# Performance work log

Hardware: AMD Instinct MI355X
Metric: run time of the kernel (lower is better)

Reference implementation:

```python
import jax, jax.numpy as jnp
import numpy as np

TOP_K = 2

def _expert(x, w1, w2, w3):
    return (jax.nn.silu(x @ w1.T) * (x @ w3.T)) @ w2.T

def setup_inputs() -> dict:
    key = jax.random.key(0)
    ks = jax.random.split(key, 8)
    B, L, D, F, E, S = 4, 2048, 1024, 512, 16, 1
    p = lambda k, shape: (jax.random.normal(k, shape, jnp.float32) * 0.02)
    return {
        "x": jax.random.normal(ks[0], (B, L, D), jnp.float32),
        "gate_w": p(ks[1], (E, D)),
        "expert_bias": jnp.zeros((E,), jnp.float32),
        "sw1": p(ks[2], (S, F, D)),
        "sw2": p(ks[3], (S, D, F)),
        "sw3": p(ks[4], (S, F, D)),
        "ew1": p(ks[5], (E, F, D)),
        "ew2": p(ks[6], (E, D, F)),
        "ew3": p(ks[7], (E, F, D)),
    }

def reference(x, gate_w, expert_bias, sw1, sw2, sw3, ew1, ew2, ew3):
    B, L, D = x.shape
    E = gate_w.shape[0]
    flat_x = x.reshape(-1, D)  # [T, D], T = B*L

    # Shared experts (always-on)
    shared = sum(_expert(flat_x, sw1[i], sw2[i], sw3[i]) for i in range(sw1.shape[0]))

    # Router (eval mode: no jitter noise, no bias update; expert_bias buffer added)
    logits = flat_x @ gate_w.T + expert_bias          # [T, E]
    probs = jax.nn.softmax(logits, axis=-1)
    topw, topi = jax.lax.top_k(probs, TOP_K)          # [T, k]
    topw = topw / jnp.sum(topw, axis=-1, keepdims=True)

    # Routed experts: combine weight per (token, expert); zero weight => zero contribution,
    # identical math to the masked gather/scatter in the original.
    out = jnp.zeros_like(flat_x)
    for e in range(E):  # fixed small structural loop over experts
        cw = jnp.sum(jnp.where(topi == e, topw, 0.0), axis=-1)  # [T]
        out = out + cw[:, None] * _expert(flat_x, ew1[e], ew2[e], ew3[e])

    y = (shared + out).reshape(B, L, D)
    return y, probs
```

## Files before the change

### kernel.cpp

```cpp
#include <hip/hip_runtime.h>

typedef unsigned short u16;
typedef __bf16 bf16_t;
typedef bf16_t bf16x8 __attribute__((ext_vector_type(8)));
typedef float f32x4 __attribute__((ext_vector_type(4)));

#define T_TOK 8192
#define DIM   1024
#define FF    512
#define NE    16
#define RBASE_SHARED (2 * T_TOK)
#define NROWS (RBASE_SHARED + T_TOK)
#define MAXTILES 256
#define NSEG 512

__device__ __forceinline__ u16 f2bf(float f) {
  union { float f; unsigned u; } v; v.f = f;
  unsigned r = v.u + 0x7FFFu + ((v.u >> 16) & 1u);
  return (u16)(r >> 16);
}
__device__ __forceinline__ float bf2f(u16 h) {
  union { unsigned u; float f; } v; v.u = ((unsigned)h) << 16; return v.f;
}
__device__ __forceinline__ int clampi(int v, int lo, int hi) {
  return v < lo ? lo : (v > hi ? hi : v);
}

#define GLL16(g, l) __builtin_amdgcn_global_load_lds( \
    (const __attribute__((address_space(1))) void*)(g), \
    (__attribute__((address_space(3))) void*)(l), 16, 0, 0)

#define X4   2097152
#define SW4  131072
#define EW4  2097152
#define TOT4 (X4 + 3 * SW4 + 3 * EW4)

__global__ __launch_bounds__(256) void cvt_all_kernel(
    const float* __restrict__ x, const float* __restrict__ sw1,
    const float* __restrict__ sw2, const float* __restrict__ sw3,
    const float* __restrict__ ew1, const float* __restrict__ ew2,
    const float* __restrict__ ew3,
    u16* __restrict__ xb, u16* __restrict__ sw1b, u16* __restrict__ sw2b,
    u16* __restrict__ sw3b, u16* __restrict__ ew1b, u16* __restrict__ ew2b,
    u16* __restrict__ ew3b) {
  int i = blockIdx.x * 256 + threadIdx.x;
  const float* s; u16* dst; int j;
  if (i < X4)                       { s = x;   dst = xb;   j = i; }
  else if (i < X4 + SW4)            { s = sw1; dst = sw1b; j = i - X4; }
  else if (i < X4 + 2 * SW4)        { s = sw2; dst = sw2b; j = i - (X4 + SW4); }
  else if (i < X4 + 3 * SW4)        { s = sw3; dst = sw3b; j = i - (X4 + 2 * SW4); }
  else if (i < X4 + 3 * SW4 + EW4)      { s = ew1; dst = ew1b; j = i - (X4 + 3 * SW4); }
  else if (i < X4 + 3 * SW4 + 2 * EW4)  { s = ew2; dst = ew2b; j = i - (X4 + 3 * SW4 + EW4); }
  else if (i < TOT4)                    { s = ew3; dst = ew3b; j = i - (X4 + 3 * SW4 + 2 * EW4); }
  else return;
  float4 v = reinterpret_cast<const float4*>(s)[j];
  ushort4 o;
  o.x = f2bf(v.x); o.y = f2bf(v.y); o.z = f2bf(v.z); o.w = f2bf(v.w);
  reinterpret_cast<ushort4*>(dst)[j] = o;
}

__global__ __launch_bounds__(256) void router_kernel(
    const float* __restrict__ x, const float* __restrict__ gw,
    const float* __restrict__ ebias, float* __restrict__ probs,
    int* __restrict__ topi, float* __restrict__ topw, int* __restrict__ cnt_seg) {
  __shared__ int hist[16];
  int tid = threadIdx.x;
  int lane = tid & 63, w = tid >> 6;
  if (tid < 16) hist[tid] = 0;
  __syncthreads();
  const float4* gv = reinterpret_cast<const float4*>(gw);
  for (int it = 0; it < 2; ++it) {
    int t0 = blockIdx.x * 16 + (w + 4 * it) * 2;
    const float4* x0 = reinterpret_cast<const float4*>(x + (size_t)t0 * DIM);
    const float4* x1 = reinterpret_cast<const float4*>(x + (size_t)(t0 + 1) * DIM);
    float4 xa[4], xc[4];
#pragma unroll
    for (int j = 0; j < 4; ++j) { xa[j] = x0[j * 64 + lane]; xc[j] = x1[j * 64 + lane]; }
    float p0[16], p1[16];
#pragma unroll
    for (int e = 0; e < NE; ++e) {
      float s0 = 0.f, s1 = 0.f;
#pragma unroll
      for (int j = 0; j < 4; ++j) {
        float4 g = gv[e * 256 + j * 64 + lane];
        s0 += xa[j].x * g.x + xa[j].y * g.y + xa[j].z * g.z + xa[j].w * g.w;
        s1 += xc[j].x * g.x + xc[j].y * g.y + xc[j].z * g.z + xc[j].w * g.w;
      }
#pragma unroll
      for (int d = 1; d < 64; d <<= 1) { s0 += __shfl_xor(s0, d); s1 += __shfl_xor(s1, d); }
      float b = ebias[e];
      p0[e] = s0 + b; p1[e] = s1 + b;
    }
    float m0 = p0[0], m1 = p1[0];
#pragma unroll
    for (int e = 1; e < NE; ++e) { m0 = fmaxf(m0, p0[e]); m1 = fmaxf(m1, p1[e]); }
    float sum0 = 0.f, sum1 = 0.f;
#pragma unroll
    for (int e = 0; e < NE; ++e) {
      p0[e] = __expf(p0[e] - m0); sum0 += p0[e];
      p1[e] = __expf(p1[e] - m1); sum1 += p1[e];
    }
    float inv0 = 1.f / sum0, inv1 = 1.f / sum1;
#pragma unroll
    for (int e = 0; e < NE; ++e) { p0[e] *= inv0; p1[e] *= inv1; }
    if (lane == 0) {
#pragma unroll
      for (int j = 0; j < 4; ++j)
        reinterpret_cast<float4*>(probs + (size_t)t0 * NE)[j] =
            make_float4(p0[4 * j], p0[4 * j + 1], p0[4 * j + 2], p0[4 * j + 3]);
      float b1 = -1.f, b2 = -1.f; int i1 = 0, i2 = 0;
#pragma unroll
      for (int e = 0; e < NE; ++e) {
        float pe = p0[e];
        if (pe > b1) { b2 = b1; i2 = i1; b1 = pe; i1 = e; }
        else if (pe > b2) { b2 = pe; i2 = e; }
      }
      float ws = b1 + b2;
      reinterpret_cast<int2*>(topi)[t0] = make_int2(i1, i2);
      reinterpret_cast<float2*>(topw)[t0] = make_float2(b1 / ws, b2 / ws);
      atomicAdd(&hist[i1], 1); atomicAdd(&hist[i2], 1);
    }
    if (lane == 1) {
      int t1 = t0 + 1;
#pragma unroll
      for (int j = 0; j < 4; ++j)
        reinterpret_cast<float4*>(probs + (size_t)t1 * NE)[j] =
            make_float4(p1[4 * j], p1[4 * j + 1], p1[4 * j + 2], p1[4 * j + 3]);
      float b1 = -1.f, b2 = -1.f; int i1 = 0, i2 = 0;
#pragma unroll
      for (int e = 0; e < NE; ++e) {
        float pe = p1[e];
        if (pe > b1) { b2 = b1; i2 = i1; b1 = pe; i1 = e; }
        else if (pe > b2) { b2 = pe; i2 = e; }
      }
      float ws = b1 + b2;
      reinterpret_cast<int2*>(topi)[t1] = make_int2(i1, i2);
      reinterpret_cast<float2*>(topw)[t1] = make_float2(b1 / ws, b2 / ws);
      atomicAdd(&hist[i1], 1); atomicAdd(&hist[i2], 1);
    }
  }
  __syncthreads();
  if (tid < 16) cnt_seg[blockIdx.x * 16 + tid] = hist[tid];
}

__global__ __launch_bounds__(256) void scan_kernel(
    const int* __restrict__ cnt_seg, int* __restrict__ cnt, int* __restrict__ offs,
    int* __restrict__ seg_base, int2* __restrict__ tab) {
  __shared__ int chunk_sum[16][16];
  __shared__ int chunk_base[16][16];
  __shared__ int tot[16], off_s[17];
  int tid = threadIdx.x;
  int e = tid & 15, c = tid >> 4;
  int s0 = 0;
  for (int s = 0; s < 32; ++s) s0 += cnt_seg[(c * 32 + s) * 16 + e];
  chunk_sum[c][e] = s0;
  __syncthreads();
  if (tid < 16) {
    int r = 0;
    for (int c2 = 0; c2 < 16; ++c2) { chunk_base[c2][tid] = r; r += chunk_sum[c2][tid]; }
    tot[tid] = r;
  }
  __syncthreads();
  if (tid == 0) {
    int a = 0;
    for (int i = 0; i < 16; ++i) { off_s[i] = a; offs[i] = a; cnt[i] = tot[i]; a += tot[i]; }
    off_s[16] = RBASE_SHARED; offs[16] = RBASE_SHARED;
    int n = 0;
    for (int g = 0; g <= 16 && n < MAXTILES; ++g) {
      int M = (g == 16) ? T_TOK : tot[g];
      for (int m0 = 0; m0 < M && n < MAXTILES; m0 += 128) { tab[n] = make_int2(g, m0); ++n; }
    }
    for (; n < MAXTILES; ++n) tab[n] = make_int2(-1, 0);
  }
  __syncthreads();
  int r = off_s[e] + chunk_base[c][e];
  for (int s = 0; s < 32; ++s) {
    int seg = c * 32 + s;
    seg_base[seg * 16 + e] = r;
    r += cnt_seg[seg * 16 + e];
  }
}

__global__ __launch_bounds__(64) void scatter_kernel(
    const int* __restrict__ topi, const float* __restrict__ topw,
    const int* __restrict__ seg_base,
    int* __restrict__ idx, float* __restrict__ cwl, int* __restrict__ slotmap) {
  __shared__ int ti[16][2]; __shared__ float tw[16][2]; __shared__ int base[16];
  int b = blockIdx.x;
  int tid = threadIdx.x;
  if (tid < 16) {
    int t = b * 16 + tid;
    int2 pp = reinterpret_cast<const int2*>(topi)[t];
    ti[tid][0] = clampi(pp.x, 0, 15); ti[tid][1] = clampi(pp.y, 0, 15);
    float2 ww = reinterpret_cast<const float2*>(topw)[t];
    tw[tid][0] = ww.x; tw[tid][1] = ww.y;
    base[tid] = seg_base[b * 16 + tid];
  }
  __syncthreads();
  if (tid < 32) {
    int l = tid >> 1, s = tid & 1;
    int t = b * 16 + l;
    int e = ti[l][s];
    int rank = 0;
    for (int t2 = 0; t2 < 16; ++t2) {
      if (ti[t2][0] == e && (t2 < l || (t2 == l && 0 < s))) ++rank;
      if (ti[t2][1] == e && (t2 < l)) ++rank;
    }
    int slot = clampi(base[e] + rank, 0, NROWS - 1);
    idx[slot] = t; cwl[slot] = tw[l][s]; slotmap[t * 3 + s] = slot;
  } else if (tid < 48) {
    int l = tid - 32;
    int t = b * 16 + l;
    int sh = RBASE_SHARED + t;
    idx[sh] = t; cwl[sh] = 1.0f; slotmap[t * 3 + 2] = sh;
  }
}

__global__ __launch_bounds__(256) void gemm_silu_kernel(
    const u16* __restrict__ A, const u16* __restrict__ sw1b, const u16* __restrict__ sw3b,
    const u16* __restrict__ ew1b, const u16* __restrict__ ew3b, u16* __restrict__ G,
    const int2* __restrict__ tab, const int* __restrict__ offs,
    const int* __restrict__ cnt, const int* __restrict__ gidx) {
  const int K = DIM;
  int2 te = tab[blockIdx.x];
  int e = te.x;
  if (e < 0) return;
  e = clampi(e, 0, NE);
  int m0 = te.y;
  int M = (e == NE) ? T_TOK : cnt[e];
  M = clampi(M, 1, T_TOK);
  int rowbase = clampi(offs[e], 0, NROWS - 1);
  const u16* B1 = (e == NE) ? sw1b : ew1b + (size_t)e * FF * K;
  const u16* B3 = (e == NE) ? sw3b : ew3b + (size_t)e * FF * K;
  int n0 = blockIdx.y * 128;

  __shared__ u16 As[128 * 32], B1s[128 * 32], B3s[128 * 32];

  int tid = threadIdx.x;
  int lane = tid & 63, wv = tid >> 6;
  int srow = tid >> 2, sg = tid & 3;
  int sk0 = (sg ^ ((srow >> 1) & 3)) * 8;
  int sk1 = (sg ^ (((srow + 64) >> 1) & 3)) * 8;
  int r0 = min(m0 + srow, M - 1);
  int r1 = min(m0 + srow + 64, M - 1);
  int ga0 = clampi(gidx[clampi(rowbase + r0, 0, NROWS - 1)], 0, T_TOK - 1);
  int ga1 = clampi(gidx[clampi(rowbase + r1, 0, NROWS - 1)], 0, T_TOK - 1);
  const u16* Ap0 = A + (size_t)ga0 * K + sk0;
  const u16* Ap1 = A + (size_t)ga1 * K + sk1;
  const u16* B1p0 = B1 + (size_t)(n0 + srow) * K + sk0;
  const u16* B1p1 = B1 + (size_t)(n0 + srow + 64) * K + sk1;
  const u16* B3p0 = B3 + (size_t)(n0 + srow) * K + sk0;
  const u16* B3p1 = B3 + (size_t)(n0 + srow + 64) * K + sk1;
  u16* lA0 = As + wv * 512;   u16* lA1 = As + 2048 + wv * 512;
  u16* lB10 = B1s + wv * 512; u16* lB11 = B1s + 2048 + wv * 512;
  u16* lB30 = B3s + wv * 512; u16* lB31 = B3s + 2048 + wv * 512;

  int ln15 = lane & 15, qd = lane >> 4;
  int qsw = (qd ^ ((ln15 >> 1) & 3)) * 8;
  int wm = (wv >> 1) * 64, wn = (wv & 1) * 64;
  int aoff = (wm + ln15) * 32 + qsw;
  int boff = (wn + ln15) * 32 + qsw;

  f32x4 acc1[4][4] = {};
  f32x4 acc3[4][4] = {};

  for (int kt = 0; kt < K; kt += 32) {
    GLL16(Ap0 + kt, lA0);   GLL16(Ap1 + kt, lA1);
    GLL16(B1p0 + kt, lB10); GLL16(B1p1 + kt, lB11);
    GLL16(B3p0 + kt, lB30); GLL16(B3p1 + kt, lB31);
    __syncthreads();
    bf16x8 af[4], b1f[4], b3f[4];
#pragma unroll
    for (int i = 0; i < 4; ++i) {
      af[i]  = *reinterpret_cast<const bf16x8*>(&As[aoff + i * 512]);
      b1f[i] = *reinterpret_cast<const bf16x8*>(&B1s[boff + i * 512]);
      b3f[i] = *reinterpret_cast<const bf16x8*>(&B3s[boff + i * 512]);
    }
#pragma unroll
    for (int i = 0; i < 4; ++i)
#pragma unroll
      for (int j = 0; j < 4; ++j) {
        acc1[i][j] = __builtin_amdgcn_mfma_f32_16x16x32_bf16(af[i], b1f[j], acc1[i][j], 0, 0, 0);
        acc3[i][j] = __builtin_amdgcn_mfma_f32_16x16x32_bf16(af[i], b3f[j], acc3[i][j], 0, 0, 0);
      }
    __syncthreads();
  }

  int mrem = M - m0;
#pragma unroll
  for (int i = 0; i < 4; ++i)
#pragma unroll
    for (int r = 0; r < 4; ++r) {
      int ml = wm + i * 16 + qd * 4 + r;
      if (ml < mrem) {
        size_t orow = (size_t)clampi(rowbase + m0 + ml, 0, NROWS - 1);
#pragma unroll
        for (int j = 0; j < 4; ++j) {
          float z1 = acc1[i][j][r], z3 = acc3[i][j][r];
          float g = z1 / (1.f + __expf(-z1)) * z3;
          G[orow * FF + n0 + wn + j * 16 + ln15] = f2bf(g);
        }
      }
    }
}

__global__ __launch_bounds__(256) void gemm_out_kernel(
    const u16* __restrict__ Gb, const u16* __restrict__ sw2b, const u16* __restrict__ ew2b,
    u16* __restrict__ O, const int2* __restrict__ tab, const int* __restrict__ offs,
    const int* __restrict__ cnt, const float* __restrict__ cwl) {
  const int K = FF;
  int2 te = tab[blockIdx.x];
  int e = te.x;
  if (e < 0) return;
  e = clampi(e, 0, NE);
  int m0 = te.y;
  int M = (e == NE) ? T_TOK : cnt[e];
  M = clampi(M, 1, T_TOK);
  int rowbase = clampi(offs[e], 0, NROWS - 1);
  const u16* B = (e == NE) ? sw2b : ew2b + (size_t)e * DIM * K;
  int n0 = blockIdx.y * 128;

  __shared__ u16 As[128 * 32], Bs[128 * 32];

  int tid = threadIdx.x;
  int lane = tid & 63, wv = tid >> 6;
  int srow = tid >> 2, sg = tid & 3;
  int sk0 = (sg ^ ((srow >> 1) & 3)) * 8;
  int sk1 = (sg ^ (((srow + 64) >> 1) & 3)) * 8;
  int r0 = clampi(rowbase + min(m0 + srow, M - 1), 0, NROWS - 1);
  int r1 = clampi(rowbase + min(m0 + srow + 64, M - 1), 0, NROWS - 1);
  const u16* Ap0 = Gb + (size_t)r0 * K + sk0;
  const u16* Ap1 = Gb + (size_t)r1 * K + sk1;
  const u16* Bp0 = B + (size_t)(n0 + srow) * K + sk0;
  const u16* Bp1 = B + (size_t)(n0 + srow + 64) * K + sk1;
  u16* lA0 = As + wv * 512; u16* lA1 = As + 2048 + wv * 512;
  u16* lB0 = Bs + wv * 512; u16* lB1 = Bs + 2048 + wv * 512;

  int ln15 = lane & 15, qd = lane >> 4;
  int qsw = (qd ^ ((ln15 >> 1) & 3)) * 8;
  int wm = (wv >> 1) * 64, wn = (wv & 1) * 64;
  int aoff = (wm + ln15) * 32 + qsw;
  int boff = (wn + ln15) * 32 + qsw;

  f32x4 acc[4][4] = {};

  for (int kt = 0; kt < K; kt += 32) {
    GLL16(Ap0 + kt, lA0); GLL16(Ap1 + kt, lA1);
    GLL16(Bp0 + kt, lB0); GLL16(Bp1 + kt, lB1);
    __syncthreads();
    bf16x8 af[4], bf[4];
#pragma unroll
    for (int i = 0; i < 4; ++i) {
      af[i] = *reinterpret_cast<const bf16x8*>(&As[aoff + i * 512]);
      bf[i] = *reinterpret_cast<const bf16x8*>(&Bs[boff + i * 512]);
    }
#pragma unroll
    for (int i = 0; i < 4; ++i)
#pragma unroll
      for (int j = 0; j < 4; ++j)
        acc[i][j] = __builtin_amdgcn_mfma_f32_16x16x32_bf16(af[i], bf[j], acc[i][j], 0, 0, 0);
    __syncthreads();
  }

  int mrem = M - m0;
#pragma unroll
  for (int i = 0; i < 4; ++i)
#pragma unroll
    for (int r = 0; r < 4; ++r) {
      int ml = wm + i * 16 + qd * 4 + r;
      if (ml < mrem) {
        int slot = clampi(rowbase + m0 + ml, 0, NROWS - 1);
        float cw = cwl[slot];
#pragma unroll
        for (int j = 0; j < 4; ++j)
          O[(size_t)slot * DIM + n0 + wn + j * 16 + ln15] = f2bf(acc[i][j][r] * cw);
      }
    }
}

__global__ __launch_bounds__(256) void combine_kernel(
    const u16* __restrict__ O, const int* __restrict__ slotmap, float* __restrict__ y) {
  int t = blockIdx.x;
  int c = threadIdx.x;
  int s0 = clampi(slotmap[t * 3], 0, NROWS - 1);
  int s1 = clampi(slotmap[t * 3 + 1], 0, NROWS - 1);
  int s2 = clampi(slotmap[t * 3 + 2], 0, NROWS - 1);
  ushort4 a = reinterpret_cast<const ushort4*>(O + (size_t)s0 * DIM)[c];
  ushort4 b = reinterpret_cast<const ushort4*>(O + (size_t)s1 * DIM)[c];
  ushort4 d = reinterpret_cast<const ushort4*>(O + (size_t)s2 * DIM)[c];
  float4 r;
  r.x = bf2f(a.x) + bf2f(b.x) + bf2f(d.x);
  r.y = bf2f(a.y) + bf2f(b.y) + bf2f(d.y);
  r.z = bf2f(a.z) + bf2f(b.z) + bf2f(d.z);
  r.w = bf2f(a.w) + bf2f(b.w) + bf2f(d.w);
  reinterpret_cast<float4*>(y + (size_t)t * DIM)[c] = r;
}

extern "C" void kernel_launch(void* const* d_in, const int* in_sizes, int n_in,
                              void* d_out, int out_size, void* d_ws, size_t ws_size,
                              hipStream_t stream) {
  const float* x     = (const float*)d_in[0];
  const float* gw    = (const float*)d_in[1];
  const float* ebias = (const float*)d_in[2];
  const float* sw1   = (const float*)d_in[3];
  const float* sw2   = (const float*)d_in[4];
  const float* sw3   = (const float*)d_in[5];
  const float* ew1   = (const float*)d_in[6];
  const float* ew2   = (const float*)d_in[7];
  const float* ew3   = (const float*)d_in[8];
  float* y = (float*)d_out;
  float* probs = y + (size_t)T_TOK * DIM;

  char* ws = (char*)d_ws;
  size_t o = 0;
  auto alloc = [&](size_t bytes) -> char* {
    char* p = ws + o;
    o = (o + bytes + 255) & ~(size_t)255;
    return p;
  };
  u16* G    = (u16*)alloc((size_t)NROWS * FF * 2);
  u16* sw1b = (u16*)alloc((size_t)FF * DIM * 2);
  u16* sw2b = (u16*)alloc((size_t)FF * DIM * 2);
  u16* sw3b = (u16*)alloc((size_t)FF * DIM * 2);
  u16* ew2b = (u16*)alloc((size_t)NE * FF * DIM * 2);
  char* aliasBase = alloc((size_t)NROWS * DIM * 2);
  u16* xb   = (u16*)aliasBase;
  u16* ew1b = (u16*)(aliasBase + (size_t)T_TOK * DIM * 2);
  u16* ew3b = (u16*)(aliasBase + (size_t)T_TOK * DIM * 2 + (size_t)NE * FF * DIM * 2);
  u16* O    = (u16*)aliasBase;
  int*   topi    = (int*)alloc(T_TOK * 2 * 4);
  float* topw    = (float*)alloc(T_TOK * 2 * 4);
  int*   idx     = (int*)alloc(NROWS * 4);
  float* cwl     = (float*)alloc(NROWS * 4);
  int*   slotmap = (int*)alloc(T_TOK * 3 * 4);
  int2*  tab     = (int2*)alloc(MAXTILES * 8);
  int*   cnt_seg = (int*)alloc(NSEG * 16 * 4);
  int*   seg_base= (int*)alloc(NSEG * 16 * 4);
  int*   cnt     = (int*)alloc(256);
  int*   offs    = (int*)alloc(256);

  router_kernel<<<NSEG, 256, 0, stream>>>(x, gw, ebias, probs, topi, topw, cnt_seg);
  scan_kernel<<<1, 256, 0, stream>>>(cnt_seg, cnt, offs, seg_base, tab);
  scatter_kernel<<<NSEG, 64, 0, stream>>>(topi, topw, seg_base, idx, cwl, slotmap);
  cvt_all_kernel<<<TOT4 / 256, 256, 0, stream>>>(x, sw1, sw2, sw3, ew1, ew2, ew3,
                                                 xb, sw1b, sw2b, sw3b, ew1b, ew2b, ew3b);

  gemm_silu_kernel<<<dim3(MAXTILES, 4, 1), 256, 0, stream>>>(
      xb, sw1b, sw3b, ew1b, ew3b, G, tab, offs, cnt, idx);
  gemm_out_kernel<<<dim3(MAXTILES, 8, 1), 256, 0, stream>>>(
      G, sw2b, ew2b, O, tab, offs, cnt, cwl);
  combine_kernel<<<T_TOK, 256, 0, stream>>>(O, slotmap, y);
}
```

Measured before the change: 457.1 us.

## Double-buffer LDS tiles and remap workgroups across XCDs in expert GEMMs

Both expert GEMM kernels now use two LDS buffers and issue the global-to-LDS loads for the next K step before computing on the current one, so load latency overlaps the MFMA work. The flat block index is also remapped so consecutive tiles are spread across the 8 XCDs, which is meant to improve L2 reuse of shared weight and activation tiles. The cost is doubled LDS per block, which may lower occupancy. The remap assumes the grid x size equals MAXTILES (256) and that the block count divides by 8, and it derives the tile and N index from the remapped id. The loop keeps one sync per iteration, and it is unclear whether that orders the prefetch writes safely against reads of the buffer they overwrite.

```diff
diff --git a/kernel.cpp b/kernel.cpp
--- a/kernel.cpp
+++ b/kernel.cpp
@@ -222,7 +222,13 @@
     const int2* __restrict__ tab, const int* __restrict__ offs,
     const int* __restrict__ cnt, const int* __restrict__ gidx) {
   const int K = DIM;
-  int2 te = tab[blockIdx.x];
+  int nwg = gridDim.x * gridDim.y;
+  int orig = blockIdx.x + gridDim.x * blockIdx.y;
+  int per = nwg >> 3;
+  int wg = (orig & 7) * per + (orig >> 3);
+  int tileid = wg & (MAXTILES - 1);
+  int ny = wg >> 8;
+  int2 te = tab[tileid];
   int e = te.x;
   if (e < 0) return;
   e = clampi(e, 0, NE);
@@ -232,9 +238,9 @@
   int rowbase = clampi(offs[e], 0, NROWS - 1);
   const u16* B1 = (e == NE) ? sw1b : ew1b + (size_t)e * FF * K;
   const u16* B3 = (e == NE) ? sw3b : ew3b + (size_t)e * FF * K;
-  int n0 = blockIdx.y * 128;
-
-  __shared__ u16 As[128 * 32], B1s[128 * 32], B3s[128 * 32];
+  int n0 = ny * 128;
+
+  __shared__ u16 As[2 * 4096], B1s[2 * 4096], B3s[2 * 4096];
 
   int tid = threadIdx.x;
   int lane = tid & 63, wv = tid >> 6;
@@ -251,9 +257,7 @@
   const u16* B1p1 = B1 + (size_t)(n0 + srow + 64) * K + sk1;
   const u16* B3p0 = B3 + (size_t)(n0 + srow) * K + sk0;
   const u16* B3p1 = B3 + (size_t)(n0 + srow + 64) * K + sk1;
-  u16* lA0 = As + wv * 512;   u16* lA1 = As + 2048 + wv * 512;
-  u16* lB10 = B1s + wv * 512; u16* lB11 = B1s + 2048 + wv * 512;
-  u16* lB30 = B3s + wv * 512; u16* lB31 = B3s + 2048 + wv * 512;
+  int st0 = wv * 512, st1 = 2048 + wv * 512;
 
   int ln15 = lane & 15, qd = lane >> 4;
   int qsw = (qd ^ ((ln15 >> 1) & 3)) * 8;
@@ -264,17 +268,27 @@
   f32x4 acc1[4][4] = {};
   f32x4 acc3[4][4] = {};
 
-  for (int kt = 0; kt < K; kt += 32) {
-    GLL16(Ap0 + kt, lA0);   GLL16(Ap1 + kt, lA1);
-    GLL16(B1p0 + kt, lB10); GLL16(B1p1 + kt, lB11);
-    GLL16(B3p0 + kt, lB30); GLL16(B3p1 + kt, lB31);
-    __syncthreads();
+  const int nk = K / 32;
+  GLL16(Ap0, As + st0);        GLL16(Ap1, As + st1);
+  GLL16(B1p0, B1s + st0);      GLL16(B1p1, B1s + st1);
+  GLL16(B3p0, B3s + st0);      GLL16(B3p1, B3s + st1);
+  __syncthreads();
+#pragma unroll 2
+  for (int t = 0; t < nk; ++t) {
+    int cur = (t & 1) * 4096;
+    if (t + 1 < nk) {
+      int nxt = ((t + 1) & 1) * 4096;
+      int kt = (t + 1) * 32;
+      GLL16(Ap0 + kt, As + nxt + st0);     GLL16(Ap1 + kt, As + nxt + st1);
+      GLL16(B1p0 + kt, B1s + nxt + st0);   GLL16(B1p1 + kt, B1s + nxt + st1);
+      GLL16(B3p0 + kt, B3s + nxt + st0);   GLL16(B3p1 + kt, B3s + nxt + st1);
+    }
     bf16x8 af[4], b1f[4], b3f[4];
 #pragma unroll
     for (int i = 0; i < 4; ++i) {
-      af[i]  = *reinterpret_cast<const bf16x8*>(&As[aoff + i * 512]);
-      b1f[i] = *reinterpret_cast<const bf16x8*>(&B1s[boff + i * 512]);
-      b3f[i] = *reinterpret_cast<const bf16x8*>(&B3s[boff + i * 512]);
+      af[i]  = *reinterpret_cast<const bf16x8*>(&As[cur + aoff + i * 512]);
+      b1f[i] = *reinterpret_cast<const bf16x8*>(&B1s[cur + boff + i * 512]);
+      b3f[i] = *reinterpret_cast<const bf16x8*>(&B3s[cur + boff + i * 512]);
     }
 #pragma unroll
     for (int i = 0; i < 4; ++i)
@@ -309,7 +323,13 @@
     u16* __restrict__ O, const int2* __restrict__ tab, const int* __restrict__ offs,
     const int* __restrict__ cnt, const float* __restrict__ cwl) {
   const int K = FF;
-  int2 te = tab[blockIdx.x];
+  int nwg = gridDim.x * gridDim.y;
+  int orig = blockIdx.x + gridDim.x * blockIdx.y;
+  int per = nwg >> 3;
+  int wg = (orig & 7) * per + (orig >> 3);
+  int tileid = wg & (MAXTILES - 1);
+  int ny = wg >> 8;
+  int2 te = tab[tileid];
   int e = te.x;
   if (e < 0) return;
   e = clampi(e, 0, NE);
@@ -318,9 +338,9 @@
   M = clampi(M, 1, T_TOK);
   int rowbase = clampi(offs[e], 0, NROWS - 1);
   const u16* B = (e == NE) ? sw2b : ew2b + (size_t)e * DIM * K;
-  int n0 = blockIdx.y * 128;
-
-  __shared__ u16 As[128 * 32], Bs[128 * 32];
+  int n0 = ny * 128;
+
+  __shared__ u16 As[2 * 4096], Bs[2 * 4096];
 
   int tid = threadIdx.x;
   int lane = tid & 63, wv = tid >> 6;
@@ -333,8 +353,7 @@
   const u16* Ap1 = Gb + (size_t)r1 * K + sk1;
   const u16* Bp0 = B + (size_t)(n0 + srow) * K + sk0;
   const u16* Bp1 = B + (size_t)(n0 + srow + 64) * K + sk1;
-  u16* lA0 = As + wv * 512; u16* lA1 = As + 2048 + wv * 512;
-  u16* lB0 = Bs + wv * 512; u16* lB1 = Bs + 2048 + wv * 512;
+  int st0 = wv * 512, st1 = 2048 + wv * 512;
 
   int ln15 = lane & 15, qd = lane >> 4;
   int qsw = (qd ^ ((ln15 >> 1) & 3)) * 8;
@@ -344,15 +363,24 @@
 
   f32x4 acc[4][4] = {};
 
-  for (int kt = 0; kt < K; kt += 32) {
-    GLL16(Ap0 + kt, lA0); GLL16(Ap1 + kt, lA1);
-    GLL16(Bp0 + kt, lB0); GLL16(Bp1 + kt, lB1);
-    __syncthreads();
+  const int nk = K / 32;
+  GLL16(Ap0, As + st0);    GLL16(Ap1, As + st1);
+  GLL16(Bp0, Bs + st0);    GLL16(Bp1, Bs + st1);
+  __syncthreads();
+#pragma unroll 2
+  for (int t = 0; t < nk; ++t) {
+    int cur = (t & 1) * 4096;
+    if (t + 1 < nk) {
+      int nxt = ((t + 1) & 1) * 4096;
+      int kt = (t + 1) * 32;
+      GLL16(Ap0 + kt, As + nxt + st0);   GLL16(Ap1 + kt, As + nxt + st1);
+      GLL16(Bp0 + kt, Bs + nxt + st0);   GLL16(Bp1 + kt, Bs + nxt + st1);
+    }
     bf16x8 af[4], bf[4];
 #pragma unroll
     for (int i = 0; i < 4; ++i) {
-      af[i] = *reinterpret_cast<const bf16x8*>(&As[aoff + i * 512]);
-      bf[i] = *reinterpret_cast<const bf16x8*>(&Bs[boff + i * 512]);
+      af[i] = *reinterpret_cast<const bf16x8*>(&As[cur + aoff + i * 512]);
+      bf[i] = *reinterpret_cast<const bf16x8*>(&Bs[cur + boff + i * 512]);
     }
 #pragma unroll
     for (int i = 0; i < 4; ++i)
```

Result: no change. 449.0 us (-1.8%).
